# Kernel optimization log

Measured on AMD Instinct MI355X. Metric: run time of the kernel, lower is better.

The kernel has to match this reference:

```python
import jax, jax.numpy as jnp
import numpy as np

BITS = 4
PACK = 32 // BITS  # 8 nibbles per int32
MASK = (1 << BITS) - 1


def _dequant_gptq(qweight, qzeros, scales):
    """GPTQ int4 dequantization matching MixedPrecisionLinear._dequantize_gptq_weight.

    qweight: [OC//PACK, IC] int32 (nibbles packed along output-channel rows)
    qzeros:  [G, IC//PACK]  int32 (nibbles packed along IC columns)
    scales:  [G, IC]        float32
    returns: [OC, IC]       float32 dequantized weight (pre-transpose)
    """
    Rp, IC = qweight.shape
    OC = Rp * PACK
    G = qzeros.shape[0]
    g = OC // G  # group size along OC

    # Unpack weights: row r*PACK + k comes from packed row r, shift k*BITS
    shifts = jnp.arange(PACK, dtype=jnp.int32) * BITS  # [PACK]
    Wq = ((qweight[:, None, :] >> shifts[None, :, None]) & MASK).reshape(OC, IC)

    # Unpack zero points per (group, ic)
    col = jnp.arange(IC, dtype=jnp.int32)
    qz_cols = qzeros[:, col // PACK]                       # [G, IC]
    zp = (qz_cols >> ((col % PACK) * BITS)[None, :]) & MASK  # [G, IC]

    zp_full = jnp.repeat(zp, g, axis=0)                    # [OC, IC]
    scales_full = jnp.repeat(scales, g, axis=0)            # [OC, IC]
    return (Wq - zp_full).astype(jnp.float32) * scales_full


def setup_inputs() -> dict:
    key = jax.random.key(0)
    k0, k1, k2, k3, k4 = jax.random.split(key, 5)
    IN, OUT, G = 4096, 11008, 32   # in_features (OC, packed), out_features (IC), groups
    N = 4096                        # flattened batch*seq tokens
    qweight = jax.random.randint(k0, (IN // PACK, OUT), 0, 2147483647, dtype=jnp.int32)
    qzeros = jax.random.randint(k1, (G, OUT // PACK), 0, 2147483647, dtype=jnp.int32)
    scales = jax.random.uniform(k2, (G, OUT), dtype=jnp.float32) * 0.01
    x = jax.random.normal(k3, (N, IN), dtype=jnp.float32)
    bias = jax.random.normal(k4, (OUT,), dtype=jnp.float32) * 0.01
    return {"input": x, "qweight": qweight, "qzeros": qzeros, "scales": scales, "bias": bias}


def reference(input, qweight, qzeros, scales, bias):
    # W_deq is [OC=in_features, IC=out_features]; the module returns W_deq.t() as the
    # linear weight, so F.linear(input, W_deq.t()) == input @ W_deq + bias.
    W = _dequant_gptq(qweight, qzeros, scales)
    return input @ W + bias
```

## Files before the change

kernel.cpp:

```cpp
#include <hip/hip_runtime.h>
#include <hip/hip_bf16.h>
#include <stdint.h>

#define M_DIM 4096
#define N_DIM 11008
#define K_DIM 4096

typedef float f32x4 __attribute__((ext_vector_type(4)));
typedef __bf16 bf16x8 __attribute__((ext_vector_type(8)));
typedef unsigned short u16x8 __attribute__((ext_vector_type(8)));
typedef unsigned short u16x4 __attribute__((ext_vector_type(4)));

typedef __attribute__((address_space(1))) const unsigned int guint;
typedef __attribute__((address_space(3))) unsigned int luint;
#define GLOAD_LDS16(g, l) \
    __builtin_amdgcn_global_load_lds((guint*)(g), (luint*)(l), 16, 0, 0)

#define WAIT_VM8() asm volatile("s_waitcnt vmcnt(8)" ::: "memory")
#define WAIT_VM4() asm volatile("s_waitcnt vmcnt(4)" ::: "memory")
#define WAIT_VM0() asm volatile("s_waitcnt vmcnt(0)" ::: "memory")

__device__ __forceinline__ unsigned short f2bf(float f) {
    union { float f; unsigned u; } v; v.f = f;
    return (unsigned short)((v.u + 0x7FFFu + ((v.u >> 16) & 1u)) >> 16);
}

__global__ void __launch_bounds__(256) cvt_x_kernel(
    const float* __restrict__ X, __hip_bfloat16* __restrict__ Y)
{
    const size_t i = ((size_t)blockIdx.x * 256 + threadIdx.x) * 8;
    f32x4 a = *reinterpret_cast<const f32x4*>(X + i);
    f32x4 b = *reinterpret_cast<const f32x4*>(X + i + 4);
    bf16x8 h;
    #pragma unroll
    for (int e = 0; e < 4; ++e) { h[e] = (__bf16)a[e]; h[e + 4] = (__bf16)b[e]; }
    *reinterpret_cast<bf16x8*>(Y + i) = h;
}

__global__ void __launch_bounds__(256) dequant_kernel(
    const int* __restrict__ QW, const int* __restrict__ QZ,
    const float* __restrict__ SC, __hip_bfloat16* __restrict__ Wt)
{
    const int n   = blockIdx.x * 64 + (threadIdx.x & 63);
    const int k64 = blockIdx.y * 4 + (threadIdx.x >> 6);
    const int g   = k64 >> 1;
    const int zp  = ((unsigned)QZ[g * (N_DIM / 8) + (n >> 3)] >> ((n & 7) << 2)) & 15;
    const float sc = SC[g * N_DIM + n];
    const float zs = (float)zp * sc;
    #pragma unroll
    for (int r = 0; r < 8; ++r) {
        const unsigned qw = (unsigned)QW[(size_t)(k64 * 8 + r) * N_DIM + n];
        bf16x8 h;
        #pragma unroll
        for (int j = 0; j < 8; ++j)
            h[j] = (__bf16)((float)((qw >> (j * 4)) & 15u) * sc - zs);
        *reinterpret_cast<bf16x8*>(Wt + (size_t)n * K_DIM + k64 * 64 + r * 8) = h;
    }
}

__global__ void __launch_bounds__(512, 2) gemm_bf16_kernel(
    const __hip_bfloat16* __restrict__ A,
    const __hip_bfloat16* __restrict__ Bt,
    const float* __restrict__ BIAS, float* __restrict__ OUT)
{
    extern __shared__ unsigned char lds[];

    const int tid  = threadIdx.x;
    const int wave = tid >> 6;
    const int lane = tid & 63;
    const int l15  = lane & 15;
    const int lhi  = lane >> 4;
    const int wr   = wave >> 2;
    const int wc   = wave & 3;

    const int bid = blockIdx.x;
    const int swz = (bid & 7) * 86 + (bid >> 3);
    const int m0  = (swz & 15) * 256;
    const int n0  = (swz >> 4) * 256;

    const int r_loc  = wave * 16 + (lane >> 2);
    const int kswz8  = ((lane & 3) ^ ((lane >> 3) & 3)) * 8;
    const __hip_bfloat16* Asrc = A  + (size_t)(m0 + r_loc) * K_DIM + kswz8;
    const __hip_bfloat16* Bsrc = Bt + (size_t)(n0 + r_loc) * K_DIM + kswz8;
    const int ldst = wave * 1024;

    const int slotx = ((lhi ^ ((l15 >> 1) & 3)) << 4);
    int aoff[8], boff[4];
    #pragma unroll
    for (int i = 0; i < 8; ++i)
        aoff[i] = (wr * 128 + i * 16 + l15) * 64 + slotx;
    #pragma unroll
    for (int j = 0; j < 4; ++j)
        boff[j] = 16384 + (wc * 64 + j * 16 + l15) * 64 + slotx;

    f32x4 acc[8][4] = {};

    auto stage = [&](int c) {
        const int buf = (c & 3) * 32768;
        const size_t kof = (size_t)c * 32;
        GLOAD_LDS16(Asrc + kof,                        lds + buf + ldst);
        GLOAD_LDS16(Asrc + kof + (size_t)128 * K_DIM,  lds + buf + 8192 + ldst);
        GLOAD_LDS16(Bsrc + kof,                        lds + buf + 16384 + ldst);
        GLOAD_LDS16(Bsrc + kof + (size_t)128 * K_DIM,  lds + buf + 16384 + 8192 + ldst);
    };

    auto compute = [&](int buf) {
        bf16x8 bfr[4], afr[4];
        #pragma unroll
        for (int j = 0; j < 4; ++j)
            bfr[j] = *reinterpret_cast<const bf16x8*>(lds + buf + boff[j]);
        #pragma unroll
        for (int i = 0; i < 4; ++i)
            afr[i] = *reinterpret_cast<const bf16x8*>(lds + buf + aoff[i]);
        __builtin_amdgcn_s_setprio(1);
        #pragma unroll
        for (int i = 0; i < 4; ++i)
            #pragma unroll
            for (int j = 0; j < 4; ++j)
                acc[i][j] = __builtin_amdgcn_mfma_f32_16x16x32_bf16(
                    afr[i], bfr[j], acc[i][j], 0, 0, 0);
        __builtin_amdgcn_s_setprio(0);
        #pragma unroll
        for (int i = 0; i < 4; ++i)
            afr[i] = *reinterpret_cast<const bf16x8*>(lds + buf + aoff[i + 4]);
        __builtin_amdgcn_s_setprio(1);
        #pragma unroll
        for (int i = 0; i < 4; ++i)
            #pragma unroll
            for (int j = 0; j < 4; ++j)
                acc[i + 4][j] = __builtin_amdgcn_mfma_f32_16x16x32_bf16(
                    afr[i], bfr[j], acc[i + 4][j], 0, 0, 0);
        __builtin_amdgcn_s_setprio(0);
    };

    stage(0); stage(1); stage(2);

    for (int c = 0; c < 125; ++c) {
        WAIT_VM8();
        __builtin_amdgcn_s_barrier();
        __builtin_amdgcn_sched_barrier(0);
        stage(c + 3);
        compute((c & 3) * 32768);
    }
    WAIT_VM8();
    __builtin_amdgcn_s_barrier();
    __builtin_amdgcn_sched_barrier(0);
    compute((125 & 3) * 32768);
    WAIT_VM4();
    __builtin_amdgcn_s_barrier();
    __builtin_amdgcn_sched_barrier(0);
    compute((126 & 3) * 32768);
    WAIT_VM0();
    __builtin_amdgcn_s_barrier();
    __builtin_amdgcn_sched_barrier(0);
    compute((127 & 3) * 32768);

    #pragma unroll
    for (int j = 0; j < 4; ++j) {
        const int n    = n0 + wc * 64 + j * 16 + l15;
        const float bv = BIAS[n];
        #pragma unroll
        for (int i = 0; i < 8; ++i) {
            const int mb = m0 + wr * 128 + i * 16 + (lhi << 2);
            #pragma unroll
            for (int t = 0; t < 4; ++t)
                OUT[(size_t)(mb + t) * N_DIM + n] = acc[i][j][t] + bv;
        }
    }
}

__global__ void __launch_bounds__(256) gptq_gemm_kernel(
    const float* __restrict__ X, const int* __restrict__ QW,
    const int* __restrict__ QZ, const float* __restrict__ SC,
    const float* __restrict__ BIAS, float* __restrict__ OUT)
{
    __shared__ __align__(16) unsigned char slds[32768];
    const int tid  = threadIdx.x;
    const int n0   = blockIdx.x * 128;
    const int m0   = blockIdx.y * 128;
    const int wave = tid >> 6;
    const int lane = tid & 63;
    const int wm   = (wave >> 1) * 64;
    const int wn   = (wave & 1) * 64;
    const int l15  = lane & 15;
    const int lhi  = lane >> 4;
    const int arow  = tid >> 4;
    const int acol4 = (tid & 15) << 2;
    const int bnl   = tid & 127;
    const int brb   = tid >> 7;
    const int col   = n0 + bnl;

    f32x4 acc[4][4] = {};
    for (int kt = 0; kt < K_DIM / 64; ++kt) {
        const int k0 = kt * 64;
        #pragma unroll
        for (int r8 = 0; r8 < 8; ++r8) {
            const int row = (r8 << 4) + arow;
            f32x4 v = *reinterpret_cast<const f32x4*>(
                X + (size_t)(m0 + row) * K_DIM + (k0 + acol4));
            u16x4 h;
            #pragma unroll
            for (int e = 0; e < 4; ++e) h[e] = f2bf(v[e]);
            const int bo = row * 128 + ((acol4 << 1) ^ ((row & 7) << 4));
            *reinterpret_cast<u16x4*>(slds + bo) = h;
        }
        {
            const int g    = k0 >> 7;
            const int zp   = (((unsigned)QZ[g * (N_DIM / 8) + (col >> 3)])
                              >> ((col & 7) << 2)) & 15;
            const float sc = SC[g * N_DIM + col];
            const float zs = (float)zp * sc;
            #pragma unroll
            for (int rb = 0; rb < 4; ++rb) {
                const int rl = (rb << 1) + brb;
                const unsigned qw =
                    (unsigned)QW[(size_t)((k0 >> 3) + rl) * N_DIM + col];
                u16x8 h;
                #pragma unroll
                for (int j = 0; j < 8; ++j) {
                    float w = (float)((qw >> (j << 2)) & 15u) * sc - zs;
                    h[j] = f2bf(w);
                }
                const int bo = 16384 + bnl * 128 + ((rl << 4) ^ ((bnl & 7) << 4));
                *reinterpret_cast<u16x8*>(slds + bo) = h;
            }
        }
        __syncthreads();
        #pragma unroll
        for (int kk = 0; kk < 2; ++kk) {
            bf16x8 afr[4], bfr[4];
            #pragma unroll
            for (int i = 0; i < 4; ++i) {
                const int row = wm + (i << 4) + l15;
                afr[i] = *reinterpret_cast<const bf16x8*>(
                    slds + row * 128 + (((kk << 6) + (lhi << 4)) ^ ((row & 7) << 4)));
            }
            #pragma unroll
            for (int j = 0; j < 4; ++j) {
                const int n = wn + (j << 4) + l15;
                bfr[j] = *reinterpret_cast<const bf16x8*>(
                    slds + 16384 + n * 128 + (((kk << 6) + (lhi << 4)) ^ ((n & 7) << 4)));
            }
            #pragma unroll
            for (int i = 0; i < 4; ++i)
                #pragma unroll
                for (int j = 0; j < 4; ++j)
                    acc[i][j] = __builtin_amdgcn_mfma_f32_16x16x32_bf16(
                        afr[i], bfr[j], acc[i][j], 0, 0, 0);
        }
        __syncthreads();
    }
    #pragma unroll
    for (int j = 0; j < 4; ++j) {
        const int n    = n0 + wn + (j << 4) + l15;
        const float bv = BIAS[n];
        #pragma unroll
        for (int i = 0; i < 4; ++i) {
            const int mb = m0 + wm + (i << 4) + (lhi << 2);
            #pragma unroll
            for (int t = 0; t < 4; ++t)
                OUT[(size_t)(mb + t) * N_DIM + n] = acc[i][j][t] + bv;
        }
    }
}

extern "C" void kernel_launch(void* const* d_in, const int* in_sizes, int n_in,
                              void* d_out, int out_size, void* d_ws, size_t ws_size,
                              hipStream_t stream) {
    const float* X  = (const float*)d_in[0];
    const int*   QW = (const int*)d_in[1];
    const int*   QZ = (const int*)d_in[2];
    const float* SC = (const float*)d_in[3];
    const float* BI = (const float*)d_in[4];
    float*      OUT = (float*)d_out;

    const size_t xbf_bytes = (size_t)M_DIM * K_DIM * 2;
    const size_t wt_bytes  = (size_t)N_DIM * K_DIM * 2;

    if (ws_size >= xbf_bytes + wt_bytes) {
        __hip_bfloat16* Xbf = (__hip_bfloat16*)d_ws;
        __hip_bfloat16* Wt  = (__hip_bfloat16*)((char*)d_ws + xbf_bytes);

        cvt_x_kernel<<<(M_DIM * K_DIM) / (256 * 8), 256, 0, stream>>>(X, Xbf);
        dequant_kernel<<<dim3(N_DIM / 64, K_DIM / 256), 256, 0, stream>>>(QW, QZ, SC, Wt);
        gemm_bf16_kernel<<<dim3((M_DIM / 256) * (N_DIM / 256)), 512, 131072, stream>>>(
            Xbf, Wt, BI, OUT);
    } else {
        gptq_gemm_kernel<<<dim3(N_DIM / 128, M_DIM / 128), 256, 0, stream>>>(
            X, QW, QZ, SC, BI, OUT);
    }
}
```

Baseline: 422.1 us.

## Restructure bf16 GEMM main loop into double-buffered 64-K tiles with interleaved staging

Replaces the four-deep ring of 32-wide K chunks with two 64-wide K buffers. Each tile is split into four MFMA quarters, and the global-to-LDS loads for the next tile are issued between them. Barriers and vmcnt waits now gate each quarter. The LDS layout also changes to a row-pair XOR swizzle with a matching read-offset formula, intended to keep LDS accesses free of bank conflicts. The aim is to overlap loads with MFMA more evenly and cut per-chunk synchronization, at the cost of more barriers per tile and a shallower prefetch depth.

```diff
diff --git a/kernel.cpp b/kernel.cpp
--- a/kernel.cpp
+++ b/kernel.cpp
@@ -19,6 +19,7 @@
 #define WAIT_VM8() asm volatile("s_waitcnt vmcnt(8)" ::: "memory")
 #define WAIT_VM4() asm volatile("s_waitcnt vmcnt(4)" ::: "memory")
 #define WAIT_VM0() asm volatile("s_waitcnt vmcnt(0)" ::: "memory")
+#define BAR()  { __builtin_amdgcn_s_barrier(); __builtin_amdgcn_sched_barrier(0); }
 
 __device__ __forceinline__ unsigned short f2bf(float f) {
     union { float f; unsigned u; } v; v.f = f;
@@ -78,93 +79,136 @@
     const int m0  = (swz & 15) * 256;
     const int n0  = (swz >> 4) * 256;
 
-    const int r_loc  = wave * 16 + (lane >> 2);
-    const int kswz8  = ((lane & 3) ^ ((lane >> 3) & 3)) * 8;
-    const __hip_bfloat16* Asrc = A  + (size_t)(m0 + r_loc) * K_DIM + kswz8;
-    const __hip_bfloat16* Bsrc = Bt + (size_t)(n0 + r_loc) * K_DIM + kswz8;
-    const int ldst = wave * 1024;
-
-    const int slotx = ((lhi ^ ((l15 >> 1) & 3)) << 4);
+    const int pp  = tid >> 3;
+    const int so  = (tid & 7) ^ (pp & 7);
+    const int grow = pp * 2 + (so >> 2);
+    const int klo  = (so & 3) * 8;
+    const __hip_bfloat16* Asrc = A  + (size_t)(m0 + grow) * K_DIM + klo;
+    const __hip_bfloat16* Bsrc = Bt + (size_t)(n0 + grow) * K_DIM + klo;
+    const int t16 = tid * 16;
+
+    const int sws   = (((l15 & 1) << 2) | lhi) ^ ((l15 >> 1) & 7);
+    const int lbase = (l15 >> 1) * 128 + sws * 16;
     int aoff[8], boff[4];
     #pragma unroll
-    for (int i = 0; i < 8; ++i)
-        aoff[i] = (wr * 128 + i * 16 + l15) * 64 + slotx;
-    #pragma unroll
-    for (int j = 0; j < 4; ++j)
-        boff[j] = 16384 + (wc * 64 + j * 16 + l15) * 64 + slotx;
+    for (int fr = 0; fr < 8; ++fr)
+        aoff[fr] = (wr * 128 + fr * 16) * 64 + lbase;
+    #pragma unroll
+    for (int fc = 0; fc < 4; ++fc)
+        boff[fc] = (wc * 64 + fc * 16) * 64 + lbase;
 
     f32x4 acc[8][4] = {};
 
-    auto stage = [&](int c) {
-        const int buf = (c & 3) * 32768;
-        const size_t kof = (size_t)c * 32;
-        GLOAD_LDS16(Asrc + kof,                        lds + buf + ldst);
-        GLOAD_LDS16(Asrc + kof + (size_t)128 * K_DIM,  lds + buf + 8192 + ldst);
-        GLOAD_LDS16(Bsrc + kof,                        lds + buf + 16384 + ldst);
-        GLOAD_LDS16(Bsrc + kof + (size_t)128 * K_DIM,  lds + buf + 16384 + 8192 + ldst);
-    };
-
-    auto compute = [&](int buf) {
-        bf16x8 bfr[4], afr[4];
-        #pragma unroll
-        for (int j = 0; j < 4; ++j)
-            bfr[j] = *reinterpret_cast<const bf16x8*>(lds + buf + boff[j]);
-        #pragma unroll
-        for (int i = 0; i < 4; ++i)
-            afr[i] = *reinterpret_cast<const bf16x8*>(lds + buf + aoff[i]);
+    auto stA0 = [&](int c) {
+        const int sb = (c & 1) * 65536; const size_t k = (size_t)c * 64;
+        GLOAD_LDS16(Asrc + k,                        lds + sb + t16);
+        GLOAD_LDS16(Asrc + k + (size_t)128 * K_DIM,  lds + sb + 8192 + t16);
+    };
+    auto stB0 = [&](int c) {
+        const int sb = (c & 1) * 65536; const size_t k = (size_t)c * 64;
+        GLOAD_LDS16(Bsrc + k,                        lds + sb + 32768 + t16);
+        GLOAD_LDS16(Bsrc + k + (size_t)128 * K_DIM,  lds + sb + 32768 + 8192 + t16);
+    };
+    auto stA1 = [&](int c) {
+        const int sb = (c & 1) * 65536; const size_t k = (size_t)c * 64 + 32;
+        GLOAD_LDS16(Asrc + k,                        lds + sb + 16384 + t16);
+        GLOAD_LDS16(Asrc + k + (size_t)128 * K_DIM,  lds + sb + 16384 + 8192 + t16);
+    };
+    auto stB1 = [&](int c) {
+        const int sb = (c & 1) * 65536; const size_t k = (size_t)c * 64 + 32;
+        GLOAD_LDS16(Bsrc + k,                        lds + sb + 49152 + t16);
+        GLOAD_LDS16(Bsrc + k + (size_t)128 * K_DIM,  lds + sb + 49152 + 8192 + t16);
+    };
+
+    auto tile = [&](int c, bool st, bool tail) {
+        const int buf = (c & 1) * 65536;
+        bf16x8 afr[4], bfr[4];
+        #pragma unroll
+        for (int fc = 0; fc < 4; ++fc)
+            bfr[fc] = *reinterpret_cast<const bf16x8*>(lds + buf + 32768 + boff[fc]);
+        #pragma unroll
+        for (int fr = 0; fr < 4; ++fr)
+            afr[fr] = *reinterpret_cast<const bf16x8*>(lds + buf + aoff[fr]);
+        if (st) stA0(c + 1);
+        BAR();
         __builtin_amdgcn_s_setprio(1);
         #pragma unroll
-        for (int i = 0; i < 4; ++i)
-            #pragma unroll
-            for (int j = 0; j < 4; ++j)
-                acc[i][j] = __builtin_amdgcn_mfma_f32_16x16x32_bf16(
-                    afr[i], bfr[j], acc[i][j], 0, 0, 0);
+        for (int fr = 0; fr < 4; ++fr)
+            #pragma unroll
+            for (int fc = 0; fc < 4; ++fc)
+                acc[fr][fc] = __builtin_amdgcn_mfma_f32_16x16x32_bf16(
+                    afr[fr], bfr[fc], acc[fr][fc], 0, 0, 0);
         __builtin_amdgcn_s_setprio(0);
-        #pragma unroll
-        for (int i = 0; i < 4; ++i)
-            afr[i] = *reinterpret_cast<const bf16x8*>(lds + buf + aoff[i + 4]);
+        BAR();
+        #pragma unroll
+        for (int fr = 0; fr < 4; ++fr)
+            afr[fr] = *reinterpret_cast<const bf16x8*>(lds + buf + aoff[fr + 4]);
+        if (st) stB0(c + 1);
+        if (tail) { WAIT_VM0(); } else { WAIT_VM4(); }
+        BAR();
         __builtin_amdgcn_s_setprio(1);
         #pragma unroll
-        for (int i = 0; i < 4; ++i)
-            #pragma unroll
-            for (int j = 0; j < 4; ++j)
-                acc[i + 4][j] = __builtin_amdgcn_mfma_f32_16x16x32_bf16(
-                    afr[i], bfr[j], acc[i + 4][j], 0, 0, 0);
+        for (int fr = 0; fr < 4; ++fr)
+            #pragma unroll
+            for (int fc = 0; fc < 4; ++fc)
+                acc[fr + 4][fc] = __builtin_amdgcn_mfma_f32_16x16x32_bf16(
+                    afr[fr], bfr[fc], acc[fr + 4][fc], 0, 0, 0);
         __builtin_amdgcn_s_setprio(0);
-    };
-
-    stage(0); stage(1); stage(2);
-
-    for (int c = 0; c < 125; ++c) {
-        WAIT_VM8();
-        __builtin_amdgcn_s_barrier();
-        __builtin_amdgcn_sched_barrier(0);
-        stage(c + 3);
-        compute((c & 3) * 32768);
-    }
+        BAR();
+        #pragma unroll
+        for (int fc = 0; fc < 4; ++fc)
+            bfr[fc] = *reinterpret_cast<const bf16x8*>(lds + buf + 49152 + boff[fc]);
+        #pragma unroll
+        for (int fr = 0; fr < 4; ++fr)
+            afr[fr] = *reinterpret_cast<const bf16x8*>(lds + buf + 16384 + aoff[fr]);
+        if (st) stA1(c + 1);
+        BAR();
+        __builtin_amdgcn_s_setprio(1);
+        #pragma unroll
+        for (int fr = 0; fr < 4; ++fr)
+            #pragma unroll
+            for (int fc = 0; fc < 4; ++fc)
+                acc[fr][fc] = __builtin_amdgcn_mfma_f32_16x16x32_bf16(
+                    afr[fr], bfr[fc], acc[fr][fc], 0, 0, 0);
+        __builtin_amdgcn_s_setprio(0);
+        BAR();
+        #pragma unroll
+        for (int fr = 0; fr < 4; ++fr)
+            afr[fr] = *reinterpret_cast<const bf16x8*>(lds + buf + 16384 + aoff[fr + 4]);
+        if (st) stB1(c + 1);
+        if (!tail) { WAIT_VM4(); }
+        BAR();
+        __builtin_amdgcn_s_setprio(1);
+        #pragma unroll
+        for (int fr = 0; fr < 4; ++fr)
+            #pragma unroll
+            for (int fc = 0; fc < 4; ++fc)
+                acc[fr + 4][fc] = __builtin_amdgcn_mfma_f32_16x16x32_bf16(
+                    afr[fr], bfr[fc], acc[fr + 4][fc], 0, 0, 0);
+        __builtin_amdgcn_s_setprio(0);
+        BAR();
+    };
+
+    stA0(0); stB0(0); stA1(0); stB1(0);
+    stA0(1); stB0(1); stA1(1); stB1(1);
     WAIT_VM8();
-    __builtin_amdgcn_s_barrier();
-    __builtin_amdgcn_sched_barrier(0);
-    compute((125 & 3) * 32768);
-    WAIT_VM4();
-    __builtin_amdgcn_s_barrier();
-    __builtin_amdgcn_sched_barrier(0);
-    compute((126 & 3) * 32768);
-    WAIT_VM0();
-    __builtin_amdgcn_s_barrier();
-    __builtin_amdgcn_sched_barrier(0);
-    compute((127 & 3) * 32768);
-
-    #pragma unroll
-    for (int j = 0; j < 4; ++j) {
-        const int n    = n0 + wc * 64 + j * 16 + l15;
+    BAR();
+
+    tile(0, false, false);
+    for (int c = 1; c <= 62; ++c)
+        tile(c, true, false);
+    tile(63, false, true);
+
+    #pragma unroll
+    for (int fc = 0; fc < 4; ++fc) {
+        const int n    = n0 + wc * 64 + fc * 16 + l15;
         const float bv = BIAS[n];
         #pragma unroll
-        for (int i = 0; i < 8; ++i) {
-            const int mb = m0 + wr * 128 + i * 16 + (lhi << 2);
+        for (int fr = 0; fr < 8; ++fr) {
+            const int mb = m0 + wr * 128 + fr * 16 + (lhi << 2);
             #pragma unroll
             for (int t = 0; t < 4; ++t)
-                OUT[(size_t)(mb + t) * N_DIM + n] = acc[i][j][t] + bv;
+                OUT[(size_t)(mb + t) * N_DIM + n] = acc[fr][fc][t] + bv;
         }
     }
 }
```

Result: no change. 425.4 us (+0.8%).
